# Kernel tuning notes

Measured on AMD Instinct MI355X. Metric: run time of the kernel, lower is better.

Reference implementation:

```python
import jax, jax.numpy as jnp
import numpy as np

B, C, H, W = 4, 256, 56, 56
K = 7
STRIDE = 1
DIL = 1
GROUPS = 16          # channels // group_channels(16)
GC = C // GROUPS     # 16 channels per group
PAD = (K + (K - 1) * (DIL - 1) - 1) // 2  # = 3
BN_EPS = 1e-5


def setup_inputs() -> dict:
    key = jax.random.key(0)
    ks = jax.random.split(key, 3)
    x = jax.random.normal(ks[0], (B, C, H, W), dtype=jnp.float32)
    # conv1: 1x1, C -> C//4, no bias (followed by BN)
    w1 = jax.random.normal(ks[1], (C // 4, C), dtype=jnp.float32) * (1.0 / np.sqrt(C))
    bn_gamma = jnp.ones((C // 4,), jnp.float32)
    bn_beta = jnp.zeros((C // 4,), jnp.float32)
    bn_mean = jnp.zeros((C // 4,), jnp.float32)
    bn_var = jnp.ones((C // 4,), jnp.float32)
    # conv2: 1x1, C//4 -> K*K*groups, with bias
    w2 = jax.random.normal(ks[2], (K * K * GROUPS, C // 4), dtype=jnp.float32) * (1.0 / np.sqrt(C // 4))
    b2 = jnp.zeros((K * K * GROUPS,), jnp.float32)
    return {"x": x, "w1": w1, "bn_gamma": bn_gamma, "bn_beta": bn_beta,
            "bn_mean": bn_mean, "bn_var": bn_var, "w2": w2, "b2": b2}


def _gen_weight(x, w1, bn_gamma, bn_beta, bn_mean, bn_var, w2, b2):
    # conv1 (1x1) + BN (inference stats) + ReLU
    h = jnp.einsum('oc,bchw->bohw', w1, x)
    scale = bn_gamma / jnp.sqrt(bn_var + BN_EPS)
    h = h * scale[None, :, None, None] + (bn_beta - bn_mean * scale)[None, :, None, None]
    h = jax.nn.relu(h)
    # conv2 (1x1) -> [B, K*K*groups, H, W]
    w = jnp.einsum('oc,bchw->bohw', w2, h) + b2[None, :, None, None]
    return w.reshape(B, GROUPS, K, K, H, W)


def _involution(x, weight):
    # x: [B,C,H,W], weight: [B,G,K,K,Ho,Wo]; stride=1 so Ho=H, Wo=W
    xp = jnp.pad(x, ((0, 0), (0, 0), (PAD, PAD), (PAD, PAD)))
    # gather K*K shifted views -> [B, C, K*K, H, W]
    patches = jnp.stack(
        [xp[:, :, i * DIL:i * DIL + H, j * DIL:j * DIL + W]
         for i in range(K) for j in range(K)], axis=2)
    patches = patches.reshape(B, GROUPS, GC, K * K, H, W)
    wflat = weight.reshape(B, GROUPS, K * K, H, W)
    out = jnp.einsum('bgckhw,bgkhw->bgchw', patches, wflat)
    return out.reshape(B, C, H, W)


def reference(x, w1, bn_gamma, bn_beta, bn_mean, bn_var, w2, b2):
    weight = _gen_weight(x, w1, bn_gamma, bn_beta, bn_mean, bn_var, w2, b2)
    return _involution(x, weight)
```

## Files before the change

kernel.cpp:

```cpp
#include <hip/hip_runtime.h>

typedef __attribute__((ext_vector_type(8))) short short8;
typedef __attribute__((ext_vector_type(4))) float f32x4;
typedef __attribute__((ext_vector_type(4))) unsigned int u32x4;
typedef unsigned short ushort_t;

#define BB 4
#define HW 3136
#define NX (4*256*3136)

#define K1_XB0 32768
#define K1_XB1 36864
#define K1_BIAS 40960
#define K1_SCV 41216
#define K1_TOT 41472

#define K2_W2P 28672
#define K2_B2S 36864
#define K2_TOT 37120

__device__ __forceinline__ unsigned int f2bf(float f) {
    unsigned int u = __float_as_uint(f);
    return (u + 0x7FFFu + ((u >> 16) & 1u)) >> 16;
}

__global__ __launch_bounds__(256) void k1_mfma(
        const float* __restrict__ x, const float* __restrict__ w1,
        const float* __restrict__ gamma, const float* __restrict__ beta,
        const float* __restrict__ mean, const float* __restrict__ var,
        ushort_t* __restrict__ h_g) {
    __shared__ __align__(16) char lds[K1_TOT];
    int blk = blockIdx.x;
    int tile = blk % 56, b = blk / 56;
    int px0 = tile * 56;
    int tid = threadIdx.x;
    int lane = tid & 63, w = tid >> 6;

    float gs = 0.f, bs = 0.f, ms = 0.f, vs = 0.f;
    if (tid < 64) { gs = gamma[tid]; bs = beta[tid]; ms = mean[tid]; vs = var[tid]; }

    int spx = tid & 63, scg = tid >> 6;
    int gpx = min(px0 + spx, HW - 1);
    const float* xbase = x + (size_t)b * 256 * HW + gpx;
    float xr[8][8];
#pragma unroll
    for (int s = 0; s < 8; s++)
#pragma unroll
        for (int u = 0; u < 8; u++)
            xr[s][u] = xbase[(size_t)(s * 32 + scg * 8 + u) * HW];

    if (tid < 64) {
        float sc = gs * rsqrtf(vs + 1e-5f);
        ((float*)(lds + K1_SCV))[tid] = sc;
        ((float*)(lds + K1_BIAS))[tid] = bs - ms * sc;
    }
    __syncthreads();

#pragma unroll
    for (int ii = 0; ii < 8; ii++) {
        int i = tid + ii * 256;
        int row = i >> 5, col8 = i & 31;
        const float* src = w1 + row * 256 + col8 * 8;
        f32x4 a = *(const f32x4*)src;
        f32x4 c = *(const f32x4*)(src + 4);
        float sc = ((const float*)(lds + K1_SCV))[row];
        unsigned int pk[4];
        pk[0] = f2bf(a[0] * sc) | (f2bf(a[1] * sc) << 16);
        pk[1] = f2bf(a[2] * sc) | (f2bf(a[3] * sc) << 16);
        pk[2] = f2bf(c[0] * sc) | (f2bf(c[1] * sc) << 16);
        pk[3] = f2bf(c[2] * sc) | (f2bf(c[3] * sc) << 16);
        u32x4 v = {pk[0], pk[1], pk[2], pk[3]};
        *(u32x4*)(lds + (row << 9) + ((col8 << 4) ^ ((row & 7) << 4))) = v;
    }

    int sdst_off = spx * 64 + ((scg << 4) ^ ((spx & 3) << 4));
    {
        unsigned int pk[4];
#pragma unroll
        for (int j = 0; j < 4; j++)
            pk[j] = f2bf(xr[0][2 * j]) | (f2bf(xr[0][2 * j + 1]) << 16);
        u32x4 v = {pk[0], pk[1], pk[2], pk[3]};
        *(u32x4*)(lds + K1_XB0 + sdst_off) = v;
    }

    f32x4 acc[4];
#pragma unroll
    for (int n = 0; n < 4; n++) acc[n] = (f32x4){0.f, 0.f, 0.f, 0.f};
    int arow = w * 16 + (lane & 15);
    int a_off = arow * 64 + (((lane >> 4) << 4) ^ ((arow & 3) << 4));

#pragma unroll
    for (int ks = 0; ks < 8; ks++) {
        __syncthreads();
        if (ks < 7) {
            unsigned int pk[4];
#pragma unroll
            for (int j = 0; j < 4; j++)
                pk[j] = f2bf(xr[ks + 1][2 * j]) | (f2bf(xr[ks + 1][2 * j + 1]) << 16);
            u32x4 v = {pk[0], pk[1], pk[2], pk[3]};
            *(u32x4*)(lds + (((ks + 1) & 1) ? K1_XB1 : K1_XB0) + sdst_off) = v;
        }
        short8 a = *(const short8*)(lds + ((ks & 1) ? K1_XB1 : K1_XB0) + a_off);
#pragma unroll
        for (int n = 0; n < 4; n++) {
            int brow = n * 16 + (lane & 15);
            short8 bb = *(const short8*)(lds + (brow << 9) +
                          ((ks * 64 + ((lane >> 4) << 4)) ^ ((brow & 7) << 4)));
            acc[n] = __builtin_amdgcn_mfma_f32_16x16x32_bf16(a, bb, acc[n], 0, 0, 0);
        }
    }

#pragma unroll
    for (int n = 0; n < 4; n++) {
        int o = n * 16 + (lane & 15);
        float bo = ((const float*)(lds + K1_BIAS))[o];
#pragma unroll
        for (int r = 0; r < 4; r++) {
            int pxl = w * 16 + ((lane >> 4) << 2) + r;
            if (pxl < 56) {
                float v = fmaxf(acc[n][r] + bo, 0.f);
                h_g[((size_t)b * HW + px0 + pxl) * 64 + o] = (ushort_t)f2bf(v);
            }
        }
    }
}

__global__ __launch_bounds__(256, 4) void k2_fused(
        const float* __restrict__ x, const ushort_t* __restrict__ h_g,
        const float* __restrict__ w2, const float* __restrict__ b2,
        float* __restrict__ out) {
    __shared__ __align__(16) char lds[K2_TOT];
    int wid0 = blockIdx.x;
    int xcd = wid0 & 7, pos = wid0 >> 3;
    int work = xcd * 112 + pos;
    int b = work / 224;
    int rem = work - b * 224;
    int half = rem / 112, r2 = rem - half * 112;
    int tloc = r2 >> 4, g = r2 & 15;
    int tile = half * 7 + tloc;
    int tid = threadIdx.x;

    const char* hg = (const char*)h_g + ((size_t)b * HW + tile * 224) * 128;
    for (int i = tid; i < 1792; i += 256) {
        int row = i >> 3, cb = (i & 7) << 4;
        u32x4 v = *(const u32x4*)(hg + row * 128 + cb);
        *(u32x4*)(lds + row * 128 + (cb ^ ((row & 7) << 4))) = v;
    }
    {
        int k = tid >> 2, cg = tid & 3;
        unsigned int pk[8];
        if (k < 49) {
            const float* wr = w2 + ((size_t)(g * 49 + k)) * 64 + cg * 16;
#pragma unroll
            for (int i = 0; i < 8; i++)
                pk[i] = f2bf(wr[2 * i]) | (f2bf(wr[2 * i + 1]) << 16);
        } else {
#pragma unroll
            for (int i = 0; i < 8; i++) pk[i] = 0;
        }
#pragma unroll
        for (int hh = 0; hh < 2; hh++) {
            u32x4 v = {pk[hh * 4 + 0], pk[hh * 4 + 1], pk[hh * 4 + 2], pk[hh * 4 + 3]};
            *(u32x4*)(lds + K2_W2P + k * 128 + ((cg * 32 + hh * 16) ^ ((k & 7) << 4))) = v;
        }
    }
    if (tid < 49) ((float*)(lds + K2_B2S))[tid] = b2[g * 49 + tid];
    __syncthreads();

    int lane = tid & 63, wd = tid >> 6;
    f32x4 acc[14];
#pragma unroll
    for (int n = 0; n < 14; n++) acc[n] = (f32x4){0.f, 0.f, 0.f, 0.f};
    int arow = wd * 16 + (lane & 15);
#pragma unroll
    for (int ks = 0; ks < 2; ks++) {
        int kc = ks * 64 + ((lane >> 4) << 4);
        short8 a = *(const short8*)(lds + K2_W2P + arow * 128 + (kc ^ ((arow & 7) << 4)));
#pragma unroll
        for (int n = 0; n < 14; n++) {
            int brow = n * 16 + (lane & 15);
            short8 bb = *(const short8*)(lds + brow * 128 + (kc ^ ((brow & 7) << 4)));
            acc[n] = __builtin_amdgcn_mfma_f32_16x16x32_bf16(a, bb, acc[n], 0, 0, 0);
        }
    }
    __syncthreads();

    {
        const float* b2s = (const float*)(lds + K2_B2S);
        ushort_t* wl = (ushort_t*)lds;
#pragma unroll
        for (int n = 0; n < 14; n++) {
#pragma unroll
            for (int rr = 0; rr < 4; rr++) {
                int tap = wd * 16 + ((lane >> 4) << 2) + rr;
                if (tap < 49) {
                    int px = n * 16 + (lane & 15);
                    wl[tap * 232 + px] = (ushort_t)f2bf(acc[n][rr] + b2s[tap]);
                }
            }
        }
    }
    __syncthreads();

    int cpk = tid >> 5;
    int pg = tid & 31;
    int py = pg >> 3, xi = pg & 7;
    if (xi < 7) {
        int x0 = xi * 8;
        int c0 = g * 16 + cpk * 2;
        int rowb = tile * 4 + py;
        float accd[2][8];
#pragma unroll
        for (int cc = 0; cc < 2; cc++)
#pragma unroll
            for (int pi = 0; pi < 8; pi++) accd[cc][pi] = 0.f;

        for (int ky = 0; ky < 7; ky++) {
            int rr = rowb + ky - 3;
            if (rr < 0 || rr >= 56) continue;
            float w[2][16];
#pragma unroll
            for (int cc = 0; cc < 2; cc++) {
                int base = (b * 256 + c0 + cc) * HW + rr * 56 + x0 - 4;
#pragma unroll
                for (int k4 = 0; k4 < 4; k4++) {
                    int o = base + k4 * 4;
                    o = min(max(o, 0), NX - 4);
                    *(f32x4*)&w[cc][k4 * 4] = *(const f32x4*)(x + o);
                }
            }
            if (x0 == 0) {
#pragma unroll
                for (int cc = 0; cc < 2; cc++) { w[cc][1] = w[cc][2] = w[cc][3] = 0.f; }
            }
            if (x0 == 48) {
#pragma unroll
                for (int cc = 0; cc < 2; cc++) { w[cc][12] = w[cc][13] = w[cc][14] = 0.f; }
            }
#pragma unroll
            for (int kx = 0; kx < 7; kx++) {
                u32x4 wv = *(const u32x4*)(lds + ((ky * 7 + kx) * 232 + py * 56 + x0) * 2);
                float wf[8];
#pragma unroll
                for (int j = 0; j < 4; j++) {
                    wf[2 * j]     = __uint_as_float(wv[j] << 16);
                    wf[2 * j + 1] = __uint_as_float(wv[j] & 0xFFFF0000u);
                }
#pragma unroll
                for (int cc = 0; cc < 2; cc++)
#pragma unroll
                    for (int pi = 0; pi < 8; pi++)
                        accd[cc][pi] = fmaf(wf[pi], w[cc][pi + kx + 1], accd[cc][pi]);
            }
        }
#pragma unroll
        for (int cc = 0; cc < 2; cc++) {
            float* op = out + (size_t)(b * 256 + c0 + cc) * HW + tile * 224 + py * 56 + x0;
            *(f32x4*)op = (f32x4){accd[cc][0], accd[cc][1], accd[cc][2], accd[cc][3]};
            *(f32x4*)(op + 4) = (f32x4){accd[cc][4], accd[cc][5], accd[cc][6], accd[cc][7]};
        }
    }
}

extern "C" void kernel_launch(void* const* d_in, const int* in_sizes, int n_in,
                              void* d_out, int out_size, void* d_ws, size_t ws_size,
                              hipStream_t stream) {
    const float* x     = (const float*)d_in[0];
    const float* w1    = (const float*)d_in[1];
    const float* gamma = (const float*)d_in[2];
    const float* beta  = (const float*)d_in[3];
    const float* mean  = (const float*)d_in[4];
    const float* var   = (const float*)d_in[5];
    const float* w2    = (const float*)d_in[6];
    const float* b2    = (const float*)d_in[7];
    float* out = (float*)d_out;

    ushort_t* h_g = (ushort_t*)d_ws;

    k1_mfma<<<224, 256, 0, stream>>>(x, w1, gamma, beta, mean, var, h_g);
    k2_fused<<<896, 256, 0, stream>>>(x, h_g, w2, b2, out);
}
```

Before: 32.38 us.

## Stage zero-padded bf16 x halo tile in LDS for involution aggregation

Before the aggregation phase, each block loads its 16-channel, 10-row x halo once from global memory, converts it to bf16 and writes it into LDS with zero padding for out-of-range rows and columns. The inner ky loop then reads x rows from LDS and drops the clamped global loads and edge-zeroing branches. The aim is to stop re-reading each x row up to seven times from global memory. The cost is more LDS per block, so launch bounds drop from 4 to 3 blocks per CU, and x is rounded to bf16, which adds precision loss.

```diff
diff --git a/kernel.cpp b/kernel.cpp
--- a/kernel.cpp
+++ b/kernel.cpp
@@ -3,6 +3,7 @@
 typedef __attribute__((ext_vector_type(8))) short short8;
 typedef __attribute__((ext_vector_type(4))) float f32x4;
 typedef __attribute__((ext_vector_type(4))) unsigned int u32x4;
+typedef __attribute__((ext_vector_type(2))) unsigned int u32x2;
 typedef unsigned short ushort_t;
 
 #define BB 4
@@ -16,8 +17,9 @@
 #define K1_TOT 41472
 
 #define K2_W2P 28672
-#define K2_B2S 36864
-#define K2_TOT 37120
+#define K2_XT  29696
+#define K2_B2S 52736
+#define K2_TOT 52944
 
 __device__ __forceinline__ unsigned int f2bf(float f) {
     unsigned int u = __float_as_uint(f);
@@ -125,7 +127,7 @@
     }
 }
 
-__global__ __launch_bounds__(256, 4) void k2_fused(
+__global__ __launch_bounds__(256, 3) void k2_fused(
         const float* __restrict__ x, const ushort_t* __restrict__ h_g,
         const float* __restrict__ w2, const float* __restrict__ b2,
         float* __restrict__ out) {
@@ -200,6 +202,28 @@
             }
         }
     }
+    {
+        int rowa0 = tile * 4 - 3;
+        const float* xg = x + ((size_t)b * 256 + g * 16) * HW;
+#pragma unroll 4
+        for (int it = 0; it < 16; it++) {
+            int p = tid + it * 256;
+            int ch = p >> 8;
+            int row = (p >> 4) & 15;
+            int q = p & 15;
+            if (row < 10) {
+                int ra = rowa0 + row;
+                unsigned int pk0 = 0, pk1 = 0;
+                if (ra >= 0 && ra < 56 && q != 0 && q != 15) {
+                    const float* src = xg + (size_t)ch * HW + ra * 56 + (q * 4 - 4);
+                    f32x4 v = *(const f32x4*)src;
+                    pk0 = f2bf(v[0]) | (f2bf(v[1]) << 16);
+                    pk1 = f2bf(v[2]) | (f2bf(v[3]) << 16);
+                }
+                *(u32x2*)(lds + K2_XT + ch * 1440 + row * 144 + q * 8) = (u32x2){pk0, pk1};
+            }
+        }
+    }
     __syncthreads();
 
     int cpk = tid >> 5;
@@ -208,34 +232,28 @@
     if (xi < 7) {
         int x0 = xi * 8;
         int c0 = g * 16 + cpk * 2;
-        int rowb = tile * 4 + py;
         float accd[2][8];
 #pragma unroll
         for (int cc = 0; cc < 2; cc++)
 #pragma unroll
             for (int pi = 0; pi < 8; pi++) accd[cc][pi] = 0.f;
 
+#pragma unroll 1
         for (int ky = 0; ky < 7; ky++) {
-            int rr = rowb + ky - 3;
-            if (rr < 0 || rr >= 56) continue;
             float w[2][16];
 #pragma unroll
             for (int cc = 0; cc < 2; cc++) {
-                int base = (b * 256 + c0 + cc) * HW + rr * 56 + x0 - 4;
-#pragma unroll
-                for (int k4 = 0; k4 < 4; k4++) {
-                    int o = base + k4 * 4;
-                    o = min(max(o, 0), NX - 4);
-                    *(f32x4*)&w[cc][k4 * 4] = *(const f32x4*)(x + o);
+                const char* xrow = lds + K2_XT + (cpk * 2 + cc) * 1440
+                                 + (py + ky) * 144 + x0 * 2;
+                u32x4 lo = *(const u32x4*)xrow;
+                u32x4 hi = *(const u32x4*)(xrow + 16);
+#pragma unroll
+                for (int j = 0; j < 4; j++) {
+                    w[cc][2 * j]     = __uint_as_float(lo[j] << 16);
+                    w[cc][2 * j + 1] = __uint_as_float(lo[j] & 0xFFFF0000u);
+                    w[cc][8 + 2 * j]     = __uint_as_float(hi[j] << 16);
+                    w[cc][8 + 2 * j + 1] = __uint_as_float(hi[j] & 0xFFFF0000u);
                 }
-            }
-            if (x0 == 0) {
-#pragma unroll
-                for (int cc = 0; cc < 2; cc++) { w[cc][1] = w[cc][2] = w[cc][3] = 0.f; }
-            }
-            if (x0 == 48) {
-#pragma unroll
-                for (int cc = 0; cc < 2; cc++) { w[cc][12] = w[cc][13] = w[cc][14] = 0.f; }
             }
 #pragma unroll
             for (int kx = 0; kx < 7; kx++) {
```

Result: slower. 44.88 us (+38.6%).
